# Performance work log

Hardware: AMD Instinct MI355X
Metric: run time of the kernel (lower is better)

The kernel has to match this reference:

```python
import jax, jax.numpy as jnp
import numpy as np

NEG_INF = -1e30


def setup_inputs() -> dict:
    key = jax.random.key(0)
    ks = jax.random.split(key, 5)
    B, S, D, H = 2, 2048, 1024, 16
    sc = 0.02  # weight init scale
    return {
        "x": jax.random.normal(ks[0], (B, S, D), dtype=jnp.float32),
        "Wq": jax.random.normal(ks[1], (D, D), dtype=jnp.float32) * sc,
        "bq": jnp.zeros((D,), dtype=jnp.float32),
        "Wk": jax.random.normal(ks[2], (D, D), dtype=jnp.float32) * sc,
        "bk": jnp.zeros((D,), dtype=jnp.float32),
        "Wv": jax.random.normal(ks[3], (D, D), dtype=jnp.float32) * sc,
        "bv": jnp.zeros((D,), dtype=jnp.float32),
        "Wo": jax.random.normal(ks[4], (D, D), dtype=jnp.float32) * sc,
        "bo": jnp.zeros((D,), dtype=jnp.float32),
        "temperature": jnp.ones((H,), dtype=jnp.float32),
    }


def reference(x, Wq, bq, Wk, bk, Wv, bv, Wo, bo, temperature):
    B, S, D = x.shape
    H = temperature.shape[0]
    hd = D // H
    sparsity = 0.8
    k = max(1, int(S * (1.0 - sparsity)))
    scale = hd ** (-0.5)

    # torch Linear: y = x @ W^T + b ; reshape to [B, S, H, hd] -> [B, H, S, hd]
    def proj(W, b):
        return (x @ W.T + b).reshape(B, S, H, hd).transpose(0, 2, 1, 3)

    q, kk, v = proj(Wq, bq), proj(Wk, bk), proj(Wv, bv)

    temp = jnp.clip(temperature, 0.1, None)[None, :, None, None]  # [1,H,1,1]
    scores = jnp.einsum("bhqd,bhkd->bhqk", q, kk) * scale / temp  # [B,H,S,S]

    # top-k sparsity: keep the k largest scores per row, -inf elsewhere.
    # Equivalent to torch's topk+scatter for distinct values: threshold at
    # the k-th largest value per row.
    topk_vals = jax.lax.top_k(scores, k)[0]           # [B,H,S,k]
    kth = topk_vals[..., -1:]                          # [B,H,S,1]
    sparse_scores = jnp.where(scores >= kth, scores, NEG_INF)

    attn = jax.nn.softmax(sparse_scores, axis=-1)      # [B,H,S,S]
    head_out = jnp.einsum("bhqk,bhkd->bhqd", attn, v)  # [B,H,S,hd]

    # stack heads back: [B,S,H,hd] -> [B,S,D], then out projection
    out = head_out.transpose(0, 2, 1, 3).reshape(B, S, D)
    out = out @ Wo.T + bo

    avg_attention = attn.mean(axis=1)                  # [B,S,S]
    return out, avg_attention
```

## Files before the change

kernel.cpp:

```cpp
#include <hip/hip_runtime.h>
#include <stdint.h>

#define S_LEN 2048
#define D_DIM 1024
#define NHEAD 16
#define HD    64
#define TOPK  409

typedef unsigned short u16;
typedef __attribute__((ext_vector_type(8))) short bf16x8;
typedef __attribute__((ext_vector_type(4))) float f32x4;
#define MFMA __builtin_amdgcn_mfma_f32_16x16x32_bf16

__device__ __forceinline__ u16 f2b(float f) {
    unsigned u = __float_as_uint(f);
    return (u16)((u + 0x7fffu + ((u >> 16) & 1u)) >> 16);
}
__device__ __forceinline__ float b2f(u16 h) {
    return __uint_as_float(((unsigned)h) << 16);
}

__global__ __launch_bounds__(256, 4)
void split_f32(const float* __restrict__ src, u16* __restrict__ hi,
               u16* __restrict__ lo, int n4)
{
    const int i = blockIdx.x * 256 + threadIdx.x;
    if (i >= n4) return;
    const float4 v = ((const float4*)src)[i];
    const float vv[4] = {v.x, v.y, v.z, v.w};
    u16 h4[4], l4[4];
#pragma unroll
    for (int c = 0; c < 4; ++c) {
        h4[c] = f2b(vv[c]);
        l4[c] = f2b(vv[c] - b2f(h4[c]));
    }
    ((ushort4*)hi)[i] = make_ushort4(h4[0], h4[1], h4[2], h4[3]);
    ((ushort4*)lo)[i] = make_ushort4(l4[0], l4[1], l4[2], l4[3]);
}

template<int MODE>
__global__ __launch_bounds__(512, 2)
void proj_mfma(const u16* __restrict__ Ahi, const u16* __restrict__ Alo,
               const u16* __restrict__ Whi, const u16* __restrict__ Wlo,
               const float* __restrict__ bias, float* __restrict__ outf,
               u16* __restrict__ o1, u16* __restrict__ o2)
{
    const int t = threadIdx.x, w = t >> 6, l = t & 63;
    const int lq = l & 15, quad = l >> 4;
    const int m0 = blockIdx.y * 128 + (w >> 2) * 64;
    const int n0 = blockIdx.x * 128 + (w & 3) * 32;

    f32x4 acc[4][2];
#pragma unroll
    for (int i = 0; i < 4; ++i)
#pragma unroll
        for (int j = 0; j < 2; ++j) acc[i][j] = (f32x4){0.f, 0.f, 0.f, 0.f};

    const size_t abase = (size_t)(m0 + lq) * D_DIM + quad * 8;
    const size_t bbase = (size_t)(n0 + lq) * D_DIM + quad * 8;

#pragma unroll 2
    for (int k0 = 0; k0 < D_DIM; k0 += 32) {
        bf16x8 ah[4], al[4], bh[2], bl[2];
#pragma unroll
        for (int i = 0; i < 4; ++i) {
            ah[i] = *(const bf16x8*)(Ahi + abase + (size_t)i * 16 * D_DIM + k0);
            al[i] = *(const bf16x8*)(Alo + abase + (size_t)i * 16 * D_DIM + k0);
        }
#pragma unroll
        for (int j = 0; j < 2; ++j) {
            bh[j] = *(const bf16x8*)(Whi + bbase + (size_t)j * 16 * D_DIM + k0);
            bl[j] = *(const bf16x8*)(Wlo + bbase + (size_t)j * 16 * D_DIM + k0);
        }
#pragma unroll
        for (int i = 0; i < 4; ++i)
#pragma unroll
            for (int j = 0; j < 2; ++j) {
                acc[i][j] = MFMA(ah[i], bh[j], acc[i][j], 0, 0, 0);
                acc[i][j] = MFMA(ah[i], bl[j], acc[i][j], 0, 0, 0);
                acc[i][j] = MFMA(al[i], bh[j], acc[i][j], 0, 0, 0);
            }
    }

#pragma unroll
    for (int j = 0; j < 2; ++j) {
        const int n = n0 + j * 16 + lq;
        const float bb = bias[n];
        const int hh = n >> 6, ee = n & 63;
#pragma unroll
        for (int i = 0; i < 4; ++i) {
            const int mb = m0 + i * 16 + quad * 4;
            const int bbm = mb >> 11, ss = mb & 2047;
            if (MODE == 2) {
#pragma unroll
                for (int r = 0; r < 4; ++r)
                    outf[(size_t)(mb + r) * D_DIM + n] = acc[i][j][r] + bb;
            } else if (MODE == 1) {
                ushort4 pk;
                pk.x = f2b(acc[i][j][0] + bb);
                pk.y = f2b(acc[i][j][1] + bb);
                pk.z = f2b(acc[i][j][2] + bb);
                pk.w = f2b(acc[i][j][3] + bb);
                *(ushort4*)(o1 + ((size_t)((bbm * NHEAD + hh) * HD + ee)) * S_LEN + ss) = pk;
            } else {
#pragma unroll
                for (int r = 0; r < 4; ++r) {
                    const float v = acc[i][j][r] + bb;
                    const size_t idx = ((size_t)(bbm * NHEAD + hh) * S_LEN + ss + r) * HD + ee;
                    const u16 h = f2b(v);
                    o1[idx] = h;
                    o2[idx] = f2b(v - b2f(h));
                }
            }
        }
    }
}

__global__ __launch_bounds__(512, 2)
void attn_mfma(const u16* __restrict__ Qhi, const u16* __restrict__ Qlo,
               const u16* __restrict__ Khi, const u16* __restrict__ Klo,
               const u16* __restrict__ Vt,  const float* __restrict__ temp,
               u16* __restrict__ HOhi, u16* __restrict__ HOlo,
               float* __restrict__ avg)
{
    __shared__ __align__(16) u16 aLds[16 * 2056];
    __shared__ float pvpart[4 * 16 * 16];
    __shared__ int   cnts[16][8][5];
    __shared__ float red[16][8][2];
    __shared__ float rowMu[16], rowSig[16], rowLo[16], rowHi[16], rowZi[16];

    const int t = threadIdx.x, w = t >> 6, l = t & 63;
    const int lq = l & 15, quad = l >> 4;
    const int b  = blockIdx.x >> 7;
    const int q0 = (blockIdx.x & 127) << 4;

    float avgreg[64];
#pragma unroll
    for (int i = 0; i < 64; ++i) avgreg[i] = 0.f;

#pragma unroll 1
    for (int h = 0; h < NHEAD; ++h) {
        const size_t bh = (size_t)(b * NHEAD + h) * S_LEN;
        const float tscale = 0.125f / fmaxf(temp[h], 0.1f);

        const u16* qph = Qhi + (bh + q0 + lq) * HD + quad * 8;
        const u16* qpl = Qlo + (bh + q0 + lq) * HD + quad * 8;
        const bf16x8 qh0 = *(const bf16x8*)qph;
        const bf16x8 qh1 = *(const bf16x8*)(qph + 32);
        const bf16x8 ql0 = *(const bf16x8*)qpl;
        const bf16x8 ql1 = *(const bf16x8*)(qpl + 32);

        f32x4 acc[16];
        const u16* kph = Khi + (bh + w * 256 + lq) * HD + quad * 8;
        const u16* kpl = Klo + (bh + w * 256 + lq) * HD + quad * 8;
#pragma unroll
        for (int tt = 0; tt < 16; ++tt) {
            const bf16x8 k0 = *(const bf16x8*)(kph + tt * 16 * HD);
            const bf16x8 k1 = *(const bf16x8*)(kph + tt * 16 * HD + 32);
            const bf16x8 m0 = *(const bf16x8*)(kpl + tt * 16 * HD);
            const bf16x8 m1 = *(const bf16x8*)(kpl + tt * 16 * HD + 32);
            f32x4 a = {0.f, 0.f, 0.f, 0.f};
            a = MFMA(qh0, k0, a, 0, 0, 0);
            a = MFMA(qh1, k1, a, 0, 0, 0);
            a = MFMA(qh0, m0, a, 0, 0, 0);
            a = MFMA(qh1, m1, a, 0, 0, 0);
            a = MFMA(ql0, k0, a, 0, 0, 0);
            a = MFMA(ql1, k1, a, 0, 0, 0);
            acc[tt] = a * tscale;
        }
        __syncthreads();

        {
            float s1[4] = {0.f,0.f,0.f,0.f}, s2[4] = {0.f,0.f,0.f,0.f};
#pragma unroll
            for (int tt = 0; tt < 16; ++tt)
#pragma unroll
                for (int r = 0; r < 4; ++r) {
                    const float v = acc[tt][r];
                    s1[r] += v;
                    s2[r] = __fmaf_rn(v, v, s2[r]);
                }
#pragma unroll
            for (int off = 1; off < 16; off <<= 1)
#pragma unroll
                for (int r = 0; r < 4; ++r) {
                    s1[r] += __shfl_xor(s1[r], off, 16);
                    s2[r] += __shfl_xor(s2[r], off, 16);
                }
            if (lq == 0)
#pragma unroll
                for (int r = 0; r < 4; ++r) {
                    red[quad * 4 + r][w][0] = s1[r];
                    red[quad * 4 + r][w][1] = s2[r];
                }
        }
        __syncthreads();
        if (t < 16) {
            float a = 0.f, c = 0.f;
#pragma unroll
            for (int ww = 0; ww < 8; ++ww) { a += red[t][ww][0]; c += red[t][ww][1]; }
            const float mu = a * (1.f / 2048.f);
            const float va = c * (1.f / 2048.f) - mu * mu;
            rowMu[t] = mu;
            rowSig[t] = sqrtf(fmaxf(va, 0.f));
        }
        __syncthreads();

        {
            float th[5][4];
            int c[5][4];
#pragma unroll
            for (int r = 0; r < 4; ++r) {
                const float mu = rowMu[quad * 4 + r], sg = rowSig[quad * 4 + r];
#pragma unroll
                for (int i = 0; i < 5; ++i) {
                    th[i][r] = __fmaf_rn(sg, 0.55f + 0.15f * (float)i, mu);
                    c[i][r] = 0;
                }
            }
#pragma unroll
            for (int tt = 0; tt < 16; ++tt)
#pragma unroll
                for (int r = 0; r < 4; ++r) {
                    const float v = acc[tt][r];
#pragma unroll
                    for (int i = 0; i < 5; ++i) c[i][r] += (v >= th[i][r]) ? 1 : 0;
                }
#pragma unroll
            for (int off = 1; off < 16; off <<= 1)
#pragma unroll
                for (int i = 0; i < 5; ++i)
#pragma unroll
                    for (int r = 0; r < 4; ++r) c[i][r] += __shfl_xor(c[i][r], off, 16);
            if (lq == 0)
#pragma unroll
                for (int r = 0; r < 4; ++r)
#pragma unroll
                    for (int i = 0; i < 5; ++i) cnts[quad * 4 + r][w][i] = c[i][r];
        }
        __syncthreads();
        if (t < 16) {
            int c[5] = {0, 0, 0, 0, 0};
#pragma unroll
            for (int ww = 0; ww < 8; ++ww)
#pragma unroll
                for (int i = 0; i < 5; ++i) c[i] += cnts[t][ww][i];
            const float mu = rowMu[t], sg = rowSig[t];
            float lo, hi;
            if (c[0] < TOPK) {
                lo = __fmaf_rn(sg, -6.f, mu);
                hi = __fmaf_rn(sg, 0.55f + 0.15f * 0.f, mu);
            } else if (c[4] >= TOPK) {
                lo = __fmaf_rn(sg, 0.55f + 0.15f * 4.f, mu);
                hi = __fmaf_rn(sg, 6.f, mu);
            } else {
                int bi = 0;
#pragma unroll
                for (int j = 1; j < 4; ++j) if (c[j] >= TOPK) bi = j;
                lo = __fmaf_rn(sg, 0.55f + 0.15f * (float)bi, mu);
                hi = __fmaf_rn(sg, 0.55f + 0.15f * (float)(bi + 1), mu);
            }
            rowLo[t] = lo;
            rowHi[t] = hi;
        }
        __syncthreads();

#pragma unroll 1
        for (int rd = 0; rd < 5; ++rd) {
            {
                float th[3][4];
                int c[3][4];
#pragma unroll
                for (int r = 0; r < 4; ++r) {
                    const float lo_ = rowLo[quad * 4 + r], hi_ = rowHi[quad * 4 + r];
                    const float w4 = __fmul_rn(__fsub_rn(hi_, lo_), 0.25f);
#pragma unroll
                    for (int j = 0; j < 3; ++j) {
                        th[j][r] = __fmaf_rn(w4, (float)(j + 1), lo_);
                        c[j][r] = 0;
                    }
                }
#pragma unroll
                for (int tt = 0; tt < 16; ++tt)
#pragma unroll
                    for (int r = 0; r < 4; ++r) {
                        const float v = acc[tt][r];
#pragma unroll
                        for (int j = 0; j < 3; ++j) c[j][r] += (v >= th[j][r]) ? 1 : 0;
                    }
#pragma unroll
                for (int off = 1; off < 16; off <<= 1)
#pragma unroll
                    for (int j = 0; j < 3; ++j)
#pragma unroll
                        for (int r = 0; r < 4; ++r) c[j][r] += __shfl_xor(c[j][r], off, 16);
                if (lq == 0)
#pragma unroll
                    for (int r = 0; r < 4; ++r)
#pragma unroll
                        for (int j = 0; j < 3; ++j) cnts[quad * 4 + r][w][j] = c[j][r];
            }
            __syncthreads();
            if (t < 16) {
                int d[3] = {0, 0, 0};
#pragma unroll
                for (int ww = 0; ww < 8; ++ww)
#pragma unroll
                    for (int j = 0; j < 3; ++j) d[j] += cnts[t][ww][j];
                float lo = rowLo[t], hi = rowHi[t];
                const float w4 = __fmul_rn(__fsub_rn(hi, lo), 0.25f);
                const float t1 = __fmaf_rn(w4, 1.f, lo);
                const float t2 = __fmaf_rn(w4, 2.f, lo);
                const float t3 = __fmaf_rn(w4, 3.f, lo);
                if (d[2] >= TOPK)      { lo = t3; }
                else if (d[1] >= TOPK) { lo = t2; hi = t3; }
                else if (d[0] >= TOPK) { lo = t1; hi = t2; }
                else                   { hi = t1; }
                rowLo[t] = lo;
                rowHi[t] = hi;
            }
            __syncthreads();
        }

        float kth[4], zp[4] = {0.f, 0.f, 0.f, 0.f};
#pragma unroll
        for (int r = 0; r < 4; ++r) kth[r] = rowLo[quad * 4 + r];
#pragma unroll
        for (int tt = 0; tt < 16; ++tt)
#pragma unroll
            for (int r = 0; r < 4; ++r) {
                const float v = acc[tt][r];
                const float e = (v >= kth[r]) ? __expf(v) : 0.f;
                acc[tt][r] = e;
                zp[r] += e;
            }
#pragma unroll
        for (int off = 1; off < 16; off <<= 1)
#pragma unroll
            for (int r = 0; r < 4; ++r) zp[r] += __shfl_xor(zp[r], off, 16);
        if (lq == 0)
#pragma unroll
            for (int r = 0; r < 4; ++r) red[quad * 4 + r][w][0] = zp[r];
        __syncthreads();
        if (t < 16) {
            float z = 0.f;
#pragma unroll
            for (int ww = 0; ww < 8; ++ww) z += red[t][ww][0];
            rowZi[t] = 1.f / z;
        }
        __syncthreads();
        float zi[4];
#pragma unroll
        for (int r = 0; r < 4; ++r) zi[r] = rowZi[quad * 4 + r];

#pragma unroll
        for (int tt = 0; tt < 16; ++tt)
#pragma unroll
            for (int r = 0; r < 4; ++r) {
                const float a_ = acc[tt][r] * zi[r];
                avgreg[tt * 4 + r] += a_;
                aLds[(quad * 4 + r) * 2056 + w * 256 + tt * 16 + lq] = f2b(a_);
            }
        __syncthreads();

        const int et = w & 3, jh = w >> 2;
        const u16* vb = Vt + ((size_t)(b * NHEAD + h) * HD + et * 16 + lq) * S_LEN
                        + jh * 1024 + quad * 8;
        const u16* ab = aLds + lq * 2056 + jh * 1024 + quad * 8;
        f32x4 pv = {0.f, 0.f, 0.f, 0.f};
#pragma unroll 8
        for (int st = 0; st < 32; ++st) {
            const bf16x8 af = *(const bf16x8*)(ab + st * 32);
            const bf16x8 vf = *(const bf16x8*)(vb + st * 32);
            pv = MFMA(af, vf, pv, 0, 0, 0);
        }
        if (w >= 4) {
#pragma unroll
            for (int r = 0; r < 4; ++r)
                pvpart[(et * 16 + quad * 4 + r) * 16 + lq] = pv[r];
        }
        __syncthreads();
        if (w < 4) {
#pragma unroll
            for (int r = 0; r < 4; ++r) {
                const float v = pv[r] + pvpart[(et * 16 + quad * 4 + r) * 16 + lq];
                const size_t idx =
                    ((size_t)(b * S_LEN + q0 + quad * 4 + r)) * D_DIM + h * HD + et * 16 + lq;
                const u16 hv = f2b(v);
                HOhi[idx] = hv;
                HOlo[idx] = f2b(v - b2f(hv));
            }
        }
    }

#pragma unroll
    for (int tt = 0; tt < 16; ++tt)
#pragma unroll
        for (int r = 0; r < 4; ++r)
            avg[((size_t)(b * S_LEN + q0 + quad * 4 + r)) * S_LEN + w * 256 + tt * 16 + lq] =
                avgreg[tt * 4 + r] * (1.f / NHEAD);
}

extern "C" void kernel_launch(void* const* d_in, const int* in_sizes, int n_in,
                              void* d_out, int out_size, void* d_ws, size_t ws_size,
                              hipStream_t stream)
{
    const float* x    = (const float*)d_in[0];
    const float* Wq   = (const float*)d_in[1];
    const float* bq   = (const float*)d_in[2];
    const float* Wk   = (const float*)d_in[3];
    const float* bk   = (const float*)d_in[4];
    const float* Wv   = (const float*)d_in[5];
    const float* bv   = (const float*)d_in[6];
    const float* Wo   = (const float*)d_in[7];
    const float* bo   = (const float*)d_in[8];
    const float* temp = (const float*)d_in[9];
    float* out = (float*)d_out;

    const int B = in_sizes[0] / (S_LEN * D_DIM);
    const int M = B * S_LEN;
    const size_t NQ = (size_t)M * D_DIM;
    const size_t NW = (size_t)D_DIM * D_DIM;

    u16* Qhi = (u16*)d_ws;
    u16* Qlo = Qhi + NQ;
    u16* Khi = Qlo + NQ;
    u16* Klo = Khi + NQ;
    u16* Vt  = Klo + NQ;
    u16* Xhi = Vt  + NQ;
    u16* Xlo = Xhi + NQ;
    u16* Wqh = Xlo + NQ;
    u16* Wql = Wqh + NW;
    u16* Wkh = Wql + NW;
    u16* Wkl = Wkh + NW;
    u16* Wvh = Wkl + NW;
    u16* Wvl = Wvh + NW;
    u16* Woh = Wvl + NW;
    u16* Wol = Woh + NW;
    float* avg = out + NQ;

    const int n4x = (int)(NQ / 4), n4w = (int)(NW / 4);
    split_f32<<<(n4x + 255) / 256, 256, 0, stream>>>(x,  Xhi, Xlo, n4x);
    split_f32<<<(n4w + 255) / 256, 256, 0, stream>>>(Wq, Wqh, Wql, n4w);
    split_f32<<<(n4w + 255) / 256, 256, 0, stream>>>(Wk, Wkh, Wkl, n4w);
    split_f32<<<(n4w + 255) / 256, 256, 0, stream>>>(Wv, Wvh, Wvl, n4w);
    split_f32<<<(n4w + 255) / 256, 256, 0, stream>>>(Wo, Woh, Wol, n4w);

    dim3 gg(D_DIM / 128, M / 128, 1);
    proj_mfma<0><<<gg, 512, 0, stream>>>(Xhi, Xlo, Wqh, Wql, bq, nullptr, Qhi, Qlo);
    proj_mfma<0><<<gg, 512, 0, stream>>>(Xhi, Xlo, Wkh, Wkl, bk, nullptr, Khi, Klo);
    proj_mfma<1><<<gg, 512, 0, stream>>>(Xhi, Xlo, Wvh, Wvl, bv, nullptr, Vt, nullptr);

    attn_mfma<<<dim3(M / 16), 512, 0, stream>>>(Qhi, Qlo, Khi, Klo, Vt, temp,
                                                Xhi, Xlo, avg);

    proj_mfma<2><<<gg, 512, 0, stream>>>(Xhi, Xlo, Woh, Wol, bo, out, nullptr, nullptr);
}
```

Baseline: 1.192 ms.

## Double attention block size and replace serial reductions with atomics and rotating buffers

Raises the attention block from 8 to 16 waves, so each wave owns 128 keys instead of 256, halving per-thread accumulator and avgreg registers. The single-thread reduction phases are replaced by LDS atomicAdd into triple-buffered count arrays and by every lane re-reducing the row statistics redundantly, which removes about half of the __syncthreads per refinement round. PV now splits the key dimension four ways and sums three partials. The aim is higher occupancy and fewer barriers, at the cost of more LDS atomics, redundant per-lane reductions, and heavier barriers across 1024 threads.

```diff
diff --git a/kernel.cpp b/kernel.cpp
--- a/kernel.cpp
+++ b/kernel.cpp
@@ -116,27 +116,31 @@
     }
 }
 
-__global__ __launch_bounds__(512, 2)
+__global__ __launch_bounds__(1024, 4)
 void attn_mfma(const u16* __restrict__ Qhi, const u16* __restrict__ Qlo,
                const u16* __restrict__ Khi, const u16* __restrict__ Klo,
                const u16* __restrict__ Vt,  const float* __restrict__ temp,
                u16* __restrict__ HOhi, u16* __restrict__ HOlo,
                float* __restrict__ avg)
 {
-    __shared__ __align__(16) u16 aLds[16 * 2056];
-    __shared__ float pvpart[4 * 16 * 16];
-    __shared__ int   cnts[16][8][5];
-    __shared__ float red[16][8][2];
-    __shared__ float rowMu[16], rowSig[16], rowLo[16], rowHi[16], rowZi[16];
+    __shared__ __align__(16) u16    aLds[16 * 2056];
+    __shared__ __align__(16) float  pvpart[3][64][17];
+    __shared__ __align__(16) int    cntb[3][16][12];
+    __shared__ __align__(16) float2 red2[16][18];
 
     const int t = threadIdx.x, w = t >> 6, l = t & 63;
     const int lq = l & 15, quad = l >> 4;
     const int b  = blockIdx.x >> 7;
     const int q0 = (blockIdx.x & 127) << 4;
 
-    float avgreg[64];
-#pragma unroll
-    for (int i = 0; i < 64; ++i) avgreg[i] = 0.f;
+    if (t < 2 * 16 * 12) ((int*)cntb)[t] = 0;
+
+    float avgreg[32];
+#pragma unroll
+    for (int i = 0; i < 32; ++i) avgreg[i] = 0.f;
+
+    int p = 0;
+    __syncthreads();
 
 #pragma unroll 1
     for (int h = 0; h < NHEAD; ++h) {
@@ -150,11 +154,11 @@
         const bf16x8 ql0 = *(const bf16x8*)qpl;
         const bf16x8 ql1 = *(const bf16x8*)(qpl + 32);
 
-        f32x4 acc[16];
-        const u16* kph = Khi + (bh + w * 256 + lq) * HD + quad * 8;
-        const u16* kpl = Klo + (bh + w * 256 + lq) * HD + quad * 8;
-#pragma unroll
-        for (int tt = 0; tt < 16; ++tt) {
+        f32x4 acc[8];
+        const u16* kph = Khi + (bh + w * 128 + lq) * HD + quad * 8;
+        const u16* kpl = Klo + (bh + w * 128 + lq) * HD + quad * 8;
+#pragma unroll
+        for (int tt = 0; tt < 8; ++tt) {
             const bf16x8 k0 = *(const bf16x8*)(kph + tt * 16 * HD);
             const bf16x8 k1 = *(const bf16x8*)(kph + tt * 16 * HD + 32);
             const bf16x8 m0 = *(const bf16x8*)(kpl + tt * 16 * HD);
@@ -168,222 +172,178 @@
             a = MFMA(ql1, k1, a, 0, 0, 0);
             acc[tt] = a * tscale;
         }
+
+#pragma unroll
+        for (int r = 0; r < 4; ++r) {
+            float s1 = 0.f, s2 = 0.f;
+#pragma unroll
+            for (int tt = 0; tt < 8; ++tt) {
+                const float v = acc[tt][r];
+                s1 += v;
+                s2 = __fmaf_rn(v, v, s2);
+            }
+#pragma unroll
+            for (int off = 1; off < 16; off <<= 1) {
+                s1 += __shfl_xor(s1, off, 16);
+                s2 += __shfl_xor(s2, off, 16);
+            }
+            if (lq == 0) red2[quad * 4 + r][w] = make_float2(s1, s2);
+        }
         __syncthreads();
-
+        float mu, sig;
         {
-            float s1[4] = {0.f,0.f,0.f,0.f}, s2[4] = {0.f,0.f,0.f,0.f};
-#pragma unroll
-            for (int tt = 0; tt < 16; ++tt)
-#pragma unroll
-                for (int r = 0; r < 4; ++r) {
-                    const float v = acc[tt][r];
-                    s1[r] += v;
-                    s2[r] = __fmaf_rn(v, v, s2[r]);
-                }
-#pragma unroll
-            for (int off = 1; off < 16; off <<= 1)
-#pragma unroll
-                for (int r = 0; r < 4; ++r) {
-                    s1[r] += __shfl_xor(s1[r], off, 16);
-                    s2[r] += __shfl_xor(s2[r], off, 16);
-                }
-            if (lq == 0)
-#pragma unroll
-                for (int r = 0; r < 4; ++r) {
-                    red[quad * 4 + r][w][0] = s1[r];
-                    red[quad * 4 + r][w][1] = s2[r];
-                }
-        }
+            float a = 0.f, c = 0.f;
+#pragma unroll
+            for (int ww = 0; ww < 8; ++ww) {
+                const float4 v = *(const float4*)&red2[lq][ww * 2];
+                a += v.x + v.z;
+                c += v.y + v.w;
+            }
+            mu = a * (1.f / 2048.f);
+            const float va = c * (1.f / 2048.f) - mu * mu;
+            sig = sqrtf(fmaxf(va, 0.f));
+        }
+
+        float muR[4], sgR[4];
+#pragma unroll
+        for (int r = 0; r < 4; ++r) {
+            muR[r] = __shfl(mu, quad * 4 + r, 16);
+            sgR[r] = __shfl(sig, quad * 4 + r, 16);
+        }
+#pragma unroll
+        for (int r = 0; r < 4; ++r)
+#pragma unroll
+            for (int i = 0; i < 5; ++i) {
+                const float th = __fmaf_rn(sgR[r], 0.55f + 0.15f * (float)i, muR[r]);
+                int c = 0;
+#pragma unroll
+                for (int tt = 0; tt < 8; ++tt) c += (acc[tt][r] >= th) ? 1 : 0;
+#pragma unroll
+                for (int off = 1; off < 16; off <<= 1) c += __shfl_xor(c, off, 16);
+                if (lq == 0) atomicAdd(&cntb[p][quad * 4 + r][i], c);
+            }
         __syncthreads();
-        if (t < 16) {
-            float a = 0.f, c = 0.f;
-#pragma unroll
-            for (int ww = 0; ww < 8; ++ww) { a += red[t][ww][0]; c += red[t][ww][1]; }
-            const float mu = a * (1.f / 2048.f);
-            const float va = c * (1.f / 2048.f) - mu * mu;
-            rowMu[t] = mu;
-            rowSig[t] = sqrtf(fmaxf(va, 0.f));
-        }
-        __syncthreads();
-
+        float lo, hi;
         {
-            float th[5][4];
-            int c[5][4];
-#pragma unroll
-            for (int r = 0; r < 4; ++r) {
-                const float mu = rowMu[quad * 4 + r], sg = rowSig[quad * 4 + r];
-#pragma unroll
-                for (int i = 0; i < 5; ++i) {
-                    th[i][r] = __fmaf_rn(sg, 0.55f + 0.15f * (float)i, mu);
-                    c[i][r] = 0;
-                }
-            }
-#pragma unroll
-            for (int tt = 0; tt < 16; ++tt)
-#pragma unroll
-                for (int r = 0; r < 4; ++r) {
-                    const float v = acc[tt][r];
-#pragma unroll
-                    for (int i = 0; i < 5; ++i) c[i][r] += (v >= th[i][r]) ? 1 : 0;
-                }
-#pragma unroll
-            for (int off = 1; off < 16; off <<= 1)
-#pragma unroll
-                for (int i = 0; i < 5; ++i)
-#pragma unroll
-                    for (int r = 0; r < 4; ++r) c[i][r] += __shfl_xor(c[i][r], off, 16);
-            if (lq == 0)
-#pragma unroll
-                for (int r = 0; r < 4; ++r)
-#pragma unroll
-                    for (int i = 0; i < 5; ++i) cnts[quad * 4 + r][w][i] = c[i][r];
-        }
-        __syncthreads();
-        if (t < 16) {
-            int c[5] = {0, 0, 0, 0, 0};
-#pragma unroll
-            for (int ww = 0; ww < 8; ++ww)
-#pragma unroll
-                for (int i = 0; i < 5; ++i) c[i] += cnts[t][ww][i];
-            const float mu = rowMu[t], sg = rowSig[t];
-            float lo, hi;
-            if (c[0] < TOPK) {
-                lo = __fmaf_rn(sg, -6.f, mu);
-                hi = __fmaf_rn(sg, 0.55f + 0.15f * 0.f, mu);
-            } else if (c[4] >= TOPK) {
-                lo = __fmaf_rn(sg, 0.55f + 0.15f * 4.f, mu);
-                hi = __fmaf_rn(sg, 6.f, mu);
+            const int4 dA = *(const int4*)&cntb[p][lq][0];
+            const int  d4 = cntb[p][lq][4];
+            const int  pz = (p == 0) ? 2 : p - 1;
+            if (t < 192) ((int*)cntb[pz])[t] = 0;
+            if (dA.x < TOPK) {
+                lo = __fmaf_rn(sig, -6.f, mu);
+                hi = __fmaf_rn(sig, 0.55f, mu);
+            } else if (d4 >= TOPK) {
+                lo = __fmaf_rn(sig, 1.15f, mu);
+                hi = __fmaf_rn(sig, 6.f, mu);
             } else {
                 int bi = 0;
-#pragma unroll
-                for (int j = 1; j < 4; ++j) if (c[j] >= TOPK) bi = j;
-                lo = __fmaf_rn(sg, 0.55f + 0.15f * (float)bi, mu);
-                hi = __fmaf_rn(sg, 0.55f + 0.15f * (float)(bi + 1), mu);
-            }
-            rowLo[t] = lo;
-            rowHi[t] = hi;
-        }
-        __syncthreads();
+                if (dA.y >= TOPK) bi = 1;
+                if (dA.z >= TOPK) bi = 2;
+                if (dA.w >= TOPK) bi = 3;
+                lo = __fmaf_rn(sig, 0.55f + 0.15f * (float)bi, mu);
+                hi = __fmaf_rn(sig, 0.70f + 0.15f * (float)bi, mu);
+            }
+            p = (p == 2) ? 0 : p + 1;
+        }
 
 #pragma unroll 1
         for (int rd = 0; rd < 5; ++rd) {
-            {
-                float th[3][4];
-                int c[3][4];
-#pragma unroll
-                for (int r = 0; r < 4; ++r) {
-                    const float lo_ = rowLo[quad * 4 + r], hi_ = rowHi[quad * 4 + r];
-                    const float w4 = __fmul_rn(__fsub_rn(hi_, lo_), 0.25f);
-#pragma unroll
-                    for (int j = 0; j < 3; ++j) {
-                        th[j][r] = __fmaf_rn(w4, (float)(j + 1), lo_);
-                        c[j][r] = 0;
-                    }
+            const float w4 = __fmul_rn(__fsub_rn(hi, lo), 0.25f);
+            float loR[4], w4R[4];
+#pragma unroll
+            for (int r = 0; r < 4; ++r) {
+                loR[r] = __shfl(lo, quad * 4 + r, 16);
+                w4R[r] = __shfl(w4, quad * 4 + r, 16);
+            }
+#pragma unroll
+            for (int r = 0; r < 4; ++r)
+#pragma unroll
+                for (int j = 0; j < 3; ++j) {
+                    const float th = __fmaf_rn(w4R[r], (float)(j + 1), loR[r]);
+                    int c = 0;
+#pragma unroll
+                    for (int tt = 0; tt < 8; ++tt) c += (acc[tt][r] >= th) ? 1 : 0;
+#pragma unroll
+                    for (int off = 1; off < 16; off <<= 1) c += __shfl_xor(c, off, 16);
+                    if (lq == 0) atomicAdd(&cntb[p][quad * 4 + r][j], c);
                 }
-#pragma unroll
-                for (int tt = 0; tt < 16; ++tt)
-#pragma unroll
-                    for (int r = 0; r < 4; ++r) {
-                        const float v = acc[tt][r];
-#pragma unroll
-                        for (int j = 0; j < 3; ++j) c[j][r] += (v >= th[j][r]) ? 1 : 0;
-                    }
-#pragma unroll
-                for (int off = 1; off < 16; off <<= 1)
-#pragma unroll
-                    for (int j = 0; j < 3; ++j)
-#pragma unroll
-                        for (int r = 0; r < 4; ++r) c[j][r] += __shfl_xor(c[j][r], off, 16);
-                if (lq == 0)
-#pragma unroll
-                    for (int r = 0; r < 4; ++r)
-#pragma unroll
-                        for (int j = 0; j < 3; ++j) cnts[quad * 4 + r][w][j] = c[j][r];
-            }
             __syncthreads();
-            if (t < 16) {
-                int d[3] = {0, 0, 0};
-#pragma unroll
-                for (int ww = 0; ww < 8; ++ww)
-#pragma unroll
-                    for (int j = 0; j < 3; ++j) d[j] += cnts[t][ww][j];
-                float lo = rowLo[t], hi = rowHi[t];
-                const float w4 = __fmul_rn(__fsub_rn(hi, lo), 0.25f);
-                const float t1 = __fmaf_rn(w4, 1.f, lo);
-                const float t2 = __fmaf_rn(w4, 2.f, lo);
-                const float t3 = __fmaf_rn(w4, 3.f, lo);
-                if (d[2] >= TOPK)      { lo = t3; }
-                else if (d[1] >= TOPK) { lo = t2; hi = t3; }
-                else if (d[0] >= TOPK) { lo = t1; hi = t2; }
-                else                   { hi = t1; }
-                rowLo[t] = lo;
-                rowHi[t] = hi;
-            }
-            __syncthreads();
-        }
-
-        float kth[4], zp[4] = {0.f, 0.f, 0.f, 0.f};
-#pragma unroll
-        for (int r = 0; r < 4; ++r) kth[r] = rowLo[quad * 4 + r];
-#pragma unroll
-        for (int tt = 0; tt < 16; ++tt)
+            const int4 dd = *(const int4*)&cntb[p][lq][0];
+            const int  pz = (p == 0) ? 2 : p - 1;
+            if (t < 192) ((int*)cntb[pz])[t] = 0;
+            const float t1 = __fmaf_rn(w4, 1.f, lo);
+            const float t2 = __fmaf_rn(w4, 2.f, lo);
+            const float t3 = __fmaf_rn(w4, 3.f, lo);
+            if (dd.z >= TOPK)      { lo = t3; }
+            else if (dd.y >= TOPK) { lo = t2; hi = t3; }
+            else if (dd.x >= TOPK) { lo = t1; hi = t2; }
+            else                   { hi = t1; }
+            p = (p == 2) ? 0 : p + 1;
+        }
+
+        float kthR[4], ziR[4];
+#pragma unroll
+        for (int r = 0; r < 4; ++r) kthR[r] = __shfl(lo, quad * 4 + r, 16);
+#pragma unroll
+        for (int r = 0; r < 4; ++r) {
+            float zp = 0.f;
+#pragma unroll
+            for (int tt = 0; tt < 8; ++tt) {
+                const float v = acc[tt][r];
+                const float e = (v >= kthR[r]) ? __expf(v) : 0.f;
+                acc[tt][r] = e;
+                zp += e;
+            }
+#pragma unroll
+            for (int off = 1; off < 16; off <<= 1) zp += __shfl_xor(zp, off, 16);
+            if (lq == 0) red2[quad * 4 + r][w].x = zp;
+        }
+        __syncthreads();
+        {
+            float z = 0.f;
+#pragma unroll
+            for (int ww = 0; ww < 8; ++ww) {
+                const float4 v = *(const float4*)&red2[lq][ww * 2];
+                z += v.x + v.z;
+            }
+            const float zi = 1.f / z;
+#pragma unroll
+            for (int r = 0; r < 4; ++r) ziR[r] = __shfl(zi, quad * 4 + r, 16);
+        }
+
+#pragma unroll
+        for (int tt = 0; tt < 8; ++tt)
 #pragma unroll
             for (int r = 0; r < 4; ++r) {
-                const float v = acc[tt][r];
-                const float e = (v >= kth[r]) ? __expf(v) : 0.f;
-                acc[tt][r] = e;
-                zp[r] += e;
-            }
-#pragma unroll
-        for (int off = 1; off < 16; off <<= 1)
-#pragma unroll
-            for (int r = 0; r < 4; ++r) zp[r] += __shfl_xor(zp[r], off, 16);
-        if (lq == 0)
-#pragma unroll
-            for (int r = 0; r < 4; ++r) red[quad * 4 + r][w][0] = zp[r];
-        __syncthreads();
-        if (t < 16) {
-            float z = 0.f;
-#pragma unroll
-            for (int ww = 0; ww < 8; ++ww) z += red[t][ww][0];
-            rowZi[t] = 1.f / z;
-        }
-        __syncthreads();
-        float zi[4];
-#pragma unroll
-        for (int r = 0; r < 4; ++r) zi[r] = rowZi[quad * 4 + r];
-
-#pragma unroll
-        for (int tt = 0; tt < 16; ++tt)
-#pragma unroll
-            for (int r = 0; r < 4; ++r) {
-                const float a_ = acc[tt][r] * zi[r];
+                const float a_ = acc[tt][r] * ziR[r];
                 avgreg[tt * 4 + r] += a_;
-                aLds[(quad * 4 + r) * 2056 + w * 256 + tt * 16 + lq] = f2b(a_);
+                aLds[(quad * 4 + r) * 2056 + w * 128 + tt * 16 + lq] = f2b(a_);
             }
         __syncthreads();
 
         const int et = w & 3, jh = w >> 2;
         const u16* vb = Vt + ((size_t)(b * NHEAD + h) * HD + et * 16 + lq) * S_LEN
-                        + jh * 1024 + quad * 8;
-        const u16* ab = aLds + lq * 2056 + jh * 1024 + quad * 8;
+                        + jh * 512 + quad * 8;
+        const u16* ab = aLds + lq * 2056 + jh * 512 + quad * 8;
         f32x4 pv = {0.f, 0.f, 0.f, 0.f};
 #pragma unroll 8
-        for (int st = 0; st < 32; ++st) {
+        for (int st = 0; st < 16; ++st) {
             const bf16x8 af = *(const bf16x8*)(ab + st * 32);
             const bf16x8 vf = *(const bf16x8*)(vb + st * 32);
             pv = MFMA(af, vf, pv, 0, 0, 0);
         }
-        if (w >= 4) {
+        if (jh > 0) {
 #pragma unroll
             for (int r = 0; r < 4; ++r)
-                pvpart[(et * 16 + quad * 4 + r) * 16 + lq] = pv[r];
+                pvpart[jh - 1][et * 16 + quad * 4 + r][lq] = pv[r];
         }
         __syncthreads();
-        if (w < 4) {
+        if (jh == 0) {
 #pragma unroll
             for (int r = 0; r < 4; ++r) {
-                const float v = pv[r] + pvpart[(et * 16 + quad * 4 + r) * 16 + lq];
+                const int row = et * 16 + quad * 4 + r;
+                const float v = pv[r] + pvpart[0][row][lq] + pvpart[1][row][lq]
+                              + pvpart[2][row][lq];
                 const size_t idx =
                     ((size_t)(b * S_LEN + q0 + quad * 4 + r)) * D_DIM + h * HD + et * 16 + lq;
                 const u16 hv = f2b(v);
@@ -394,10 +354,10 @@
     }
 
 #pragma unroll
-    for (int tt = 0; tt < 16; ++tt)
+    for (int tt = 0; tt < 8; ++tt)
 #pragma unroll
         for (int r = 0; r < 4; ++r)
-            avg[((size_t)(b * S_LEN + q0 + quad * 4 + r)) * S_LEN + w * 256 + tt * 16 + lq] =
+            avg[((size_t)(b * S_LEN + q0 + quad * 4 + r)) * S_LEN + w * 128 + tt * 16 + lq] =
                 avgreg[tt * 4 + r] * (1.f / NHEAD);
 }
 
@@ -451,8 +411,8 @@
     proj_mfma<0><<<gg, 512, 0, stream>>>(Xhi, Xlo, Wkh, Wkl, bk, nullptr, Khi, Klo);
     proj_mfma<1><<<gg, 512, 0, stream>>>(Xhi, Xlo, Wvh, Wvl, bv, nullptr, Vt, nullptr);
 
-    attn_mfma<<<dim3(M / 16), 512, 0, stream>>>(Qhi, Qlo, Khi, Klo, Vt, temp,
-                                                Xhi, Xlo, avg);
+    attn_mfma<<<dim3(M / 16), 1024, 0, stream>>>(Qhi, Qlo, Khi, Klo, Vt, temp,
+                                                 Xhi, Xlo, avg);
 
     proj_mfma<2><<<gg, 512, 0, stream>>>(Xhi, Xlo, Woh, Wol, bo, out, nullptr, nullptr);
 }
```

New measurement: 1.281 ms. 1.08x slower.
